# Kernel tuning notes

Measured on AMD Instinct MI355X. Metric: run time of the kernel, lower is better.

The kernel has to match this reference:

```python
import jax, jax.numpy as jnp
import numpy as np

B, S, D, UNITS = 64, 2048, 1024, 1024


def setup_inputs() -> dict:
    key = jax.random.key(0)
    ks = jax.random.split(key, 5)
    sc = 1.0 / np.sqrt(D)
    return {
        "s_prev": jax.random.normal(ks[0], (B, D), jnp.float32),
        "hidden_states": jax.random.normal(ks[1], (B, S, D), jnp.float32),
        "W_kernel": jax.random.normal(ks[2], (D, UNITS), jnp.float32) * sc,
        "W_bias": jnp.zeros((UNITS,), jnp.float32),
        "U_kernel": jax.random.normal(ks[3], (D, UNITS), jnp.float32) * sc,
        "U_bias": jnp.zeros((UNITS,), jnp.float32),
        "V_kernel": jax.random.normal(ks[4], (UNITS, 1), jnp.float32) * (1.0 / np.sqrt(UNITS)),
        "V_bias": jnp.zeros((1,), jnp.float32),
    }


def reference(s_prev, hidden_states, W_kernel, W_bias, U_kernel, U_bias, V_kernel, V_bias):
    # W(s_prev): [B, units], broadcast over seq axis
    w_s = (s_prev @ W_kernel + W_bias)[:, None, :]          # [B, 1, units]
    u_h = jnp.einsum('bsd,du->bsu', hidden_states, U_kernel) + U_bias  # [B, S, units]
    scores = jnp.tanh(w_s + u_h) @ V_kernel + V_bias        # [B, S, 1]
    weight = jax.nn.softmax(scores, axis=1)                 # [B, S, 1]
    context = jnp.sum(hidden_states * weight, axis=1)       # [B, D]
    return (context, weight)
```

## Files before the change

### kernel.cpp

```cpp
#include <hip/hip_runtime.h>
#include <stdint.h>

#define NB 64
#define NS 2048
#define ND 1024
#define NU 1024

typedef __attribute__((ext_vector_type(8))) _Float16 f16x8;
typedef __attribute__((ext_vector_type(4))) float f32x4;

__device__ __forceinline__ void gload_lds16(const void* g, void* l) {
    __builtin_amdgcn_global_load_lds(
        (const __attribute__((address_space(1))) unsigned int*)g,
        (__attribute__((address_space(3))) unsigned int*)l, 16, 0, 0);
}

__global__ void transpose_u(const float* __restrict__ Uk, _Float16* __restrict__ Ut) {
    __shared__ float tile[64][65];
    int d0 = blockIdx.x * 64, u0 = blockIdx.y * 64;
    int tid = threadIdx.x;
    #pragma unroll
    for (int i = 0; i < 16; ++i) {
        int idx = i * 256 + tid;
        int r = idx >> 6, c = idx & 63;
        tile[r][c] = Uk[(size_t)(d0 + r) * NU + (u0 + c)];
    }
    __syncthreads();
    #pragma unroll
    for (int i = 0; i < 16; ++i) {
        int idx = i * 256 + tid;
        int c = idx >> 6, r = idx & 63;
        Ut[(size_t)(u0 + c) * ND + (d0 + r)] = (_Float16)tile[r][c];
    }
}

__global__ void prep_off(const float* __restrict__ s_prev, const float* __restrict__ Wk,
                         const float* __restrict__ Wb, const float* __restrict__ Ub,
                         float* __restrict__ off) {
    int blk = blockIdx.x;
    int b = blk >> 2, ut = blk & 3;
    int tid = threadIdx.x;
    int u = ut * 256 + tid;
    __shared__ float sp[ND];
    #pragma unroll
    for (int i = tid; i < ND; i += 256) sp[i] = s_prev[(size_t)b * ND + i];
    __syncthreads();
    float acc = 0.f;
    #pragma unroll 8
    for (int d = 0; d < ND; ++d) acc += sp[d] * Wk[(size_t)d * NU + u];
    off[(size_t)b * NU + u] = acc + Wb[u] + Ub[u];
}

__launch_bounds__(256, 4)
__global__ void scores_kernel(const float* __restrict__ h,
                              const _Float16* __restrict__ Ut,
                              const float* __restrict__ off,
                              const float* __restrict__ V,
                              float* __restrict__ scores)
{
    int hw = blockIdx.x;
    int chunk = gridDim.x >> 3;
    int logical = (hw & 7) * chunk + (hw >> 3);
    int ublk = logical & 7;
    int t2 = logical >> 3;
    int sblk = t2 & 15;
    int b = t2 >> 4;
    int s0 = sblk * 128, u0 = ublk * 128;

    __shared__ _Float16 As[2][128][32];
    __shared__ _Float16 Bs[3][128][32];

    int tid = threadIdx.x;
    int w = tid >> 6, l = tid & 63;
    int wr = w >> 1, wc = w & 1;
    int rg = l >> 4, cl = l & 15;

    f32x4 acc[4][4] = {};

    const float* hA = h + ((size_t)b * NS + s0) * ND;

    int arow = tid >> 3;
    int acol4 = (tid & 7) * 4;
    int aslog = (tid & 7) >> 1;
    int ahalf = tid & 1;
    const _Float16* srcB[2];
    #pragma unroll
    for (int i = 0; i < 2; ++i) {
        int row = w * 32 + i * 16 + (l >> 2);
        srcB[i] = Ut + (size_t)(u0 + row) * ND + (((l & 3) ^ ((row >> 1) & 3)) * 8);
    }

    float4 av[4];

    #define LOADA(KK) { \
        _Pragma("unroll") \
        for (int p = 0; p < 4; ++p) \
            av[p] = *(const float4*)(hA + (size_t)(p * 32 + arow) * ND + (KK) * 32 + acol4); \
    }

    #define ISSUEB(BI, KK) { \
        _Pragma("unroll") \
        for (int i = 0; i < 2; ++i) \
            gload_lds16((const void*)(srcB[i] + (KK) * 32), (void*)&Bs[BI][w * 32 + i * 16][0]); \
    }

    #define CVTW(ABUF) { \
        _Pragma("unroll") \
        for (int p = 0; p < 4; ++p) { \
            int r_ = p * 32 + arow; \
            int sp_ = aslog ^ ((r_ >> 1) & 3); \
            union { _Float16 e[4]; uint2 u2; } cv; \
            cv.e[0] = (_Float16)av[p].x; cv.e[1] = (_Float16)av[p].y; \
            cv.e[2] = (_Float16)av[p].z; cv.e[3] = (_Float16)av[p].w; \
            *(uint2*)&As[ABUF][r_][sp_ * 8 + ahalf * 4] = cv.u2; \
        } \
    }

    #define COMPUTE(ABUF, BI) { \
        f16x8 af[4], bf[4]; \
        _Pragma("unroll") \
        for (int m = 0; m < 4; ++m) { \
            int r_ = wr * 64 + m * 16 + cl; \
            af[m] = *(const f16x8*)&As[ABUF][r_][(rg ^ ((r_ >> 1) & 3)) * 8]; \
        } \
        _Pragma("unroll") \
        for (int n = 0; n < 4; ++n) { \
            int r_ = wc * 64 + n * 16 + cl; \
            bf[n] = *(const f16x8*)&Bs[BI][r_][(rg ^ ((r_ >> 1) & 3)) * 8]; \
        } \
        _Pragma("unroll") \
        for (int m = 0; m < 4; ++m) \
            _Pragma("unroll") \
            for (int n = 0; n < 4; ++n) \
                acc[m][n] = __builtin_amdgcn_mfma_f32_16x16x32_f16(af[m], bf[n], acc[m][n], 0, 0, 0); \
    }

    LOADA(0);
    ISSUEB(0, 0);

    int bcur = 0;
    for (int t = 0; t < 31; ++t) {
        asm volatile("s_waitcnt vmcnt(2)" ::: "memory");
        __builtin_amdgcn_sched_barrier(0);
        CVTW(t & 1);
        LOADA(t + 1);
        int bnxt = bcur + 1; if (bnxt == 3) bnxt = 0;
        ISSUEB(bnxt, t + 1);
        asm volatile("s_waitcnt vmcnt(6) lgkmcnt(0)" ::: "memory");
        __builtin_amdgcn_sched_barrier(0);
        __builtin_amdgcn_s_barrier();
        __builtin_amdgcn_sched_barrier(0);
        COMPUTE(t & 1, bcur);
        bcur = bnxt;
    }
    asm volatile("s_waitcnt vmcnt(0)" ::: "memory");
    __builtin_amdgcn_sched_barrier(0);
    CVTW(1);
    asm volatile("s_waitcnt lgkmcnt(0)" ::: "memory");
    __builtin_amdgcn_sched_barrier(0);
    __builtin_amdgcn_s_barrier();
    __builtin_amdgcn_sched_barrier(0);
    COMPUTE(1, bcur);

    #undef LOADA
    #undef ISSUEB
    #undef CVTW
    #undef COMPUTE

    float offv[4], vv[4];
    #pragma unroll
    for (int n = 0; n < 4; ++n) {
        int u = u0 + wc * 64 + n * 16 + cl;
        offv[n] = off[(size_t)b * NU + u];
        vv[n] = V[u];
    }
    #pragma unroll
    for (int m = 0; m < 4; ++m) {
        #pragma unroll
        for (int i = 0; i < 4; ++i) {
            float sacc = 0.f;
            #pragma unroll
            for (int n = 0; n < 4; ++n) {
                float x = acc[m][n][i] + offv[n];
                float t = 1.0f - 2.0f / (1.0f + __expf(2.0f * x));
                sacc += t * vv[n];
            }
            #pragma unroll
            for (int msk = 1; msk < 16; msk <<= 1) sacc += __shfl_xor(sacc, msk, 64);
            if (cl == 0)
                atomicAdd(&scores[(size_t)b * NS + s0 + wr * 64 + m * 16 + rg * 4 + i], sacc);
        }
    }
}

__global__ void softmax_kernel(const float* __restrict__ scores, float* __restrict__ outw) {
    int b = blockIdx.x, tid = threadIdx.x;
    const float* src = scores + (size_t)b * NS;
    float4 x0 = *(const float4*)(src + tid * 8);
    float4 x1 = *(const float4*)(src + tid * 8 + 4);
    float m = fmaxf(fmaxf(fmaxf(x0.x, x0.y), fmaxf(x0.z, x0.w)),
                    fmaxf(fmaxf(x1.x, x1.y), fmaxf(x1.z, x1.w)));
    #pragma unroll
    for (int msk = 1; msk < 64; msk <<= 1) m = fmaxf(m, __shfl_xor(m, msk, 64));
    __shared__ float redm[4], reds[4];
    if ((tid & 63) == 0) redm[tid >> 6] = m;
    __syncthreads();
    m = fmaxf(fmaxf(redm[0], redm[1]), fmaxf(redm[2], redm[3]));
    float e[8];
    e[0] = __expf(x0.x - m); e[1] = __expf(x0.y - m); e[2] = __expf(x0.z - m); e[3] = __expf(x0.w - m);
    e[4] = __expf(x1.x - m); e[5] = __expf(x1.y - m); e[6] = __expf(x1.z - m); e[7] = __expf(x1.w - m);
    float s = e[0] + e[1] + e[2] + e[3] + e[4] + e[5] + e[6] + e[7];
    #pragma unroll
    for (int msk = 1; msk < 64; msk <<= 1) s += __shfl_xor(s, msk, 64);
    if ((tid & 63) == 0) reds[tid >> 6] = s;
    __syncthreads();
    float Z = reds[0] + reds[1] + reds[2] + reds[3];
    float r = 1.0f / Z;
    float4 o0 = { e[0] * r, e[1] * r, e[2] * r, e[3] * r };
    float4 o1 = { e[4] * r, e[5] * r, e[6] * r, e[7] * r };
    *(float4*)(outw + (size_t)b * NS + tid * 8) = o0;
    *(float4*)(outw + (size_t)b * NS + tid * 8 + 4) = o1;
}

__global__ void context_partial(const float* __restrict__ h, const float* __restrict__ wgt,
                                float* __restrict__ part) {
    int sc = blockIdx.x, b = blockIdx.y, tid = threadIdx.x;
    __shared__ float lw[128];
    if (tid < 128) lw[tid] = wgt[(size_t)b * NS + sc * 128 + tid];
    __syncthreads();
    const float* hb = h + ((size_t)b * NS + sc * 128) * ND + tid * 4;
    float4 acc = { 0.f, 0.f, 0.f, 0.f };
    #pragma unroll 4
    for (int s = 0; s < 128; ++s) {
        float4 hv = *(const float4*)(hb + (size_t)s * ND);
        float wv = lw[s];
        acc.x += hv.x * wv; acc.y += hv.y * wv; acc.z += hv.z * wv; acc.w += hv.w * wv;
    }
    *(float4*)(part + ((size_t)(sc * NB + b)) * ND + tid * 4) = acc;
}

__global__ void context_reduce(const float* __restrict__ part, float* __restrict__ outc) {
    int b = blockIdx.x, tid = threadIdx.x;
    float4 acc = { 0.f, 0.f, 0.f, 0.f };
    #pragma unroll
    for (int k = 0; k < 16; ++k) {
        float4 p = *(const float4*)(part + ((size_t)(k * NB + b)) * ND + tid * 4);
        acc.x += p.x; acc.y += p.y; acc.z += p.z; acc.w += p.w;
    }
    *(float4*)(outc + (size_t)b * ND + tid * 4) = acc;
}

extern "C" void kernel_launch(void* const* d_in, const int* in_sizes, int n_in,
                              void* d_out, int out_size, void* d_ws, size_t ws_size,
                              hipStream_t stream) {
    const float* s_prev = (const float*)d_in[0];
    const float* hidden = (const float*)d_in[1];
    const float* Wk     = (const float*)d_in[2];
    const float* Wb     = (const float*)d_in[3];
    const float* Uk     = (const float*)d_in[4];
    const float* Ub     = (const float*)d_in[5];
    const float* Vk     = (const float*)d_in[6];

    float* out_ctx = (float*)d_out;
    float* out_w   = out_ctx + NB * ND;

    char* ws = (char*)d_ws;
    _Float16* Ut  = (_Float16*)ws;
    float* off    = (float*)(ws + (size_t)(2 << 20));
    float* scores = (float*)(ws + (size_t)(2 << 20) + (256 << 10));
    float* part   = (float*)(ws + (size_t)(2 << 20) + (768 << 10));

    hipMemsetAsync(scores, 0, (size_t)NB * NS * sizeof(float), stream);
    transpose_u<<<dim3(16, 16), 256, 0, stream>>>(Uk, Ut);
    prep_off<<<256, 256, 0, stream>>>(s_prev, Wk, Wb, Ub, off);
    scores_kernel<<<8192, 256, 0, stream>>>(hidden, Ut, off, Vk, scores);
    softmax_kernel<<<NB, 256, 0, stream>>>(scores, out_w);
    context_partial<<<dim3(16, NB), 256, 0, stream>>>(hidden, out_w, part);
    context_reduce<<<NB, 256, 0, stream>>>(part, out_ctx);
}
```

Measured before the change: 578.1 us.

## Pre-convert hidden states to fp16 and feed scores and context from it

Adds a pass that converts the whole hidden-state tensor to fp16 in workspace. A new scores kernel then streams both A and B tiles into LDS with direct global-to-LDS loads, and a new context kernel reads the fp16 copy. The aim is to halve the bytes read by the scores GEMM and the context pass. In exchange it adds a full extra read-and-write pass over the large tensor. The new GEMM loop is single-buffered with two barriers per k-step, and the context sum loses precision because it now uses fp16 inputs. The path only runs if the workspace is large enough to hold the fp16 copy.

```diff
diff --git a/kernel.cpp b/kernel.cpp
--- a/kernel.cpp
+++ b/kernel.cpp
@@ -7,12 +7,28 @@
 #define NU 1024
 
 typedef __attribute__((ext_vector_type(8))) _Float16 f16x8;
+typedef __attribute__((ext_vector_type(4))) _Float16 f16x4;
 typedef __attribute__((ext_vector_type(4))) float f32x4;
 
 __device__ __forceinline__ void gload_lds16(const void* g, void* l) {
     __builtin_amdgcn_global_load_lds(
         (const __attribute__((address_space(1))) unsigned int*)g,
         (__attribute__((address_space(3))) unsigned int*)l, 16, 0, 0);
+}
+
+__global__ void convert_h(const float* __restrict__ h, _Float16* __restrict__ hf, size_t n8) {
+    size_t i = (size_t)blockIdx.x * blockDim.x + threadIdx.x;
+    size_t stride = (size_t)gridDim.x * blockDim.x;
+    for (; i < n8; i += stride) {
+        const float4* p = (const float4*)(h + i * 8);
+        float4 a = p[0], b = p[1];
+        union { _Float16 e[8]; uint4 v; } o;
+        o.e[0] = (_Float16)a.x; o.e[1] = (_Float16)a.y;
+        o.e[2] = (_Float16)a.z; o.e[3] = (_Float16)a.w;
+        o.e[4] = (_Float16)b.x; o.e[5] = (_Float16)b.y;
+        o.e[6] = (_Float16)b.z; o.e[7] = (_Float16)b.w;
+        *(uint4*)(hf + i * 8) = o.v;
+    }
 }
 
 __global__ void transpose_u(const float* __restrict__ Uk, _Float16* __restrict__ Ut) {
@@ -49,6 +65,96 @@
     #pragma unroll 8
     for (int d = 0; d < ND; ++d) acc += sp[d] * Wk[(size_t)d * NU + u];
     off[(size_t)b * NU + u] = acc + Wb[u] + Ub[u];
+}
+
+__launch_bounds__(256, 4)
+__global__ void scores_f16(const _Float16* __restrict__ hf,
+                           const _Float16* __restrict__ Ut,
+                           const float* __restrict__ off,
+                           const float* __restrict__ V,
+                           float* __restrict__ scores)
+{
+    int hw = blockIdx.x;
+    int chunk = gridDim.x >> 3;
+    int logical = (hw & 7) * chunk + (hw >> 3);
+    int ublk = logical & 7;
+    int t2 = logical >> 3;
+    int sblk = t2 & 15;
+    int b = t2 >> 4;
+    int s0 = sblk * 128, u0 = ublk * 128;
+
+    __shared__ _Float16 As[128][32];
+    __shared__ _Float16 Bs[128][32];
+
+    int tid = threadIdx.x;
+    int w = tid >> 6, l = tid & 63;
+    int wr = w >> 1, wc = w & 1;
+    int rg = l >> 4, cl = l & 15;
+
+    f32x4 acc[4][4] = {};
+
+    const _Float16* srcA[2];
+    const _Float16* srcB[2];
+    #pragma unroll
+    for (int i = 0; i < 2; ++i) {
+        int row = w * 32 + i * 16 + (l >> 2);
+        int gs = ((l & 3) ^ ((row >> 1) & 3)) * 8;
+        srcA[i] = hf + ((size_t)b * NS + s0 + row) * ND + gs;
+        srcB[i] = Ut + (size_t)(u0 + row) * ND + gs;
+    }
+
+    for (int kk = 0; kk < 32; ++kk) {
+        int k0 = kk * 32;
+        __syncthreads();
+        #pragma unroll
+        for (int i = 0; i < 2; ++i) {
+            gload_lds16((const void*)(srcA[i] + k0), (void*)&As[w * 32 + i * 16][0]);
+            gload_lds16((const void*)(srcB[i] + k0), (void*)&Bs[w * 32 + i * 16][0]);
+        }
+        __syncthreads();
+
+        f16x8 af[4], bf[4];
+        #pragma unroll
+        for (int m = 0; m < 4; ++m) {
+            int r_ = wr * 64 + m * 16 + cl;
+            af[m] = *(const f16x8*)&As[r_][(rg ^ ((r_ >> 1) & 3)) * 8];
+        }
+        #pragma unroll
+        for (int n = 0; n < 4; ++n) {
+            int r_ = wc * 64 + n * 16 + cl;
+            bf[n] = *(const f16x8*)&Bs[r_][(rg ^ ((r_ >> 1) & 3)) * 8];
+        }
+        #pragma unroll
+        for (int m = 0; m < 4; ++m)
+            #pragma unroll
+            for (int n = 0; n < 4; ++n)
+                acc[m][n] = __builtin_amdgcn_mfma_f32_16x16x32_f16(af[m], bf[n], acc[m][n], 0, 0, 0);
+    }
+
+    float offv[4], vv[4];
+    #pragma unroll
+    for (int n = 0; n < 4; ++n) {
+        int u = u0 + wc * 64 + n * 16 + cl;
+        offv[n] = off[(size_t)b * NU + u];
+        vv[n] = V[u];
+    }
+    #pragma unroll
+    for (int m = 0; m < 4; ++m) {
+        #pragma unroll
+        for (int i = 0; i < 4; ++i) {
+            float sacc = 0.f;
+            #pragma unroll
+            for (int n = 0; n < 4; ++n) {
+                float x = acc[m][n][i] + offv[n];
+                float t = 1.0f - 2.0f / (1.0f + __expf(2.0f * x));
+                sacc += t * vv[n];
+            }
+            #pragma unroll
+            for (int msk = 1; msk < 16; msk <<= 1) sacc += __shfl_xor(sacc, msk, 64);
+            if (cl == 0)
+                atomicAdd(&scores[(size_t)b * NS + s0 + wr * 64 + m * 16 + rg * 4 + i], sacc);
+        }
+    }
 }
 
 __launch_bounds__(256, 4)
@@ -78,7 +184,6 @@
     f32x4 acc[4][4] = {};
 
     const float* hA = h + ((size_t)b * NS + s0) * ND;
-
     int arow = tid >> 3;
     int acol4 = (tid & 7) * 4;
     int aslog = (tid & 7) >> 1;
@@ -97,13 +202,11 @@
         for (int p = 0; p < 4; ++p) \
             av[p] = *(const float4*)(hA + (size_t)(p * 32 + arow) * ND + (KK) * 32 + acol4); \
     }
-
     #define ISSUEB(BI, KK) { \
         _Pragma("unroll") \
         for (int i = 0; i < 2; ++i) \
             gload_lds16((const void*)(srcB[i] + (KK) * 32), (void*)&Bs[BI][w * 32 + i * 16][0]); \
     }
-
     #define CVTW(ABUF) { \
         _Pragma("unroll") \
         for (int p = 0; p < 4; ++p) { \
@@ -115,7 +218,6 @@
             *(uint2*)&As[ABUF][r_][sp_ * 8 + ahalf * 4] = cv.u2; \
         } \
     }
-
     #define COMPUTE(ABUF, BI) { \
         f16x8 af[4], bf[4]; \
         _Pragma("unroll") \
@@ -137,7 +239,6 @@
 
     LOADA(0);
     ISSUEB(0, 0);
-
     int bcur = 0;
     for (int t = 0; t < 31; ++t) {
         asm volatile("s_waitcnt vmcnt(2)" ::: "memory");
@@ -222,6 +323,24 @@
     *(float4*)(outw + (size_t)b * NS + tid * 8 + 4) = o1;
 }
 
+__global__ void context_partial_f16(const _Float16* __restrict__ hf, const float* __restrict__ wgt,
+                                    float* __restrict__ part) {
+    int sc = blockIdx.x, b = blockIdx.y, tid = threadIdx.x;
+    __shared__ float lw[128];
+    if (tid < 128) lw[tid] = wgt[(size_t)b * NS + sc * 128 + tid];
+    __syncthreads();
+    const _Float16* hb = hf + ((size_t)b * NS + sc * 128) * ND + tid * 4;
+    float4 acc = { 0.f, 0.f, 0.f, 0.f };
+    #pragma unroll 4
+    for (int s = 0; s < 128; ++s) {
+        f16x4 hv = *(const f16x4*)(hb + (size_t)s * ND);
+        float wv = lw[s];
+        acc.x += (float)hv[0] * wv; acc.y += (float)hv[1] * wv;
+        acc.z += (float)hv[2] * wv; acc.w += (float)hv[3] * wv;
+    }
+    *(float4*)(part + ((size_t)(sc * NB + b)) * ND + tid * 4) = acc;
+}
+
 __global__ void context_partial(const float* __restrict__ h, const float* __restrict__ wgt,
                                 float* __restrict__ part) {
     int sc = blockIdx.x, b = blockIdx.y, tid = threadIdx.x;
@@ -269,12 +388,26 @@
     float* off    = (float*)(ws + (size_t)(2 << 20));
     float* scores = (float*)(ws + (size_t)(2 << 20) + (256 << 10));
     float* part   = (float*)(ws + (size_t)(2 << 20) + (768 << 10));
+    size_t small  = (size_t)(2 << 20) + (768 << 10) + (4 << 20);
+    _Float16* hf16 = (_Float16*)(ws + small);
+    size_t hbytes = (size_t)NB * NS * ND * sizeof(_Float16);
+
+    bool fast = (ws_size >= small + hbytes);
 
     hipMemsetAsync(scores, 0, (size_t)NB * NS * sizeof(float), stream);
     transpose_u<<<dim3(16, 16), 256, 0, stream>>>(Uk, Ut);
     prep_off<<<256, 256, 0, stream>>>(s_prev, Wk, Wb, Ub, off);
-    scores_kernel<<<8192, 256, 0, stream>>>(hidden, Ut, off, Vk, scores);
-    softmax_kernel<<<NB, 256, 0, stream>>>(scores, out_w);
-    context_partial<<<dim3(16, NB), 256, 0, stream>>>(hidden, out_w, part);
+
+    if (fast) {
+        size_t n8 = (size_t)NB * NS * ND / 8;
+        convert_h<<<8192, 256, 0, stream>>>(hidden, hf16, n8);
+        scores_f16<<<8192, 256, 0, stream>>>(hf16, Ut, off, Vk, scores);
+        softmax_kernel<<<NB, 256, 0, stream>>>(scores, out_w);
+        context_partial_f16<<<dim3(16, NB), 256, 0, stream>>>(hf16, out_w, part);
+    } else {
+        scores_kernel<<<8192, 256, 0, stream>>>(hidden, Ut, off, Vk, scores);
+        softmax_kernel<<<NB, 256, 0, stream>>>(scores, out_w);
+        context_partial<<<dim3(16, NB), 256, 0, stream>>>(hidden, out_w, part);
+    }
     context_reduce<<<NB, 256, 0, stream>>>(part, out_ctx);
 }
```

After: 610.4 us. 5.6% more time.
